# Performance work log

Measured on AMD Instinct MI355X. Metric: run time of the kernel, lower is better.

The kernel has to match this reference:

```python
import jax, jax.numpy as jnp
import numpy as np

DIM = 1024
HEADS = 8
SCALE = 64 ** (-0.5)  # module uses dimHead=64 even though per-head c = DIM//HEADS = 128
LN_EPS = 1e-3  # keras LayerNormalization default


def _layernorm(t, g, b):
    mu = jnp.mean(t, axis=-1, keepdims=True)
    var = jnp.mean(jnp.square(t - mu), axis=-1, keepdims=True)
    return (t - mu) * jax.lax.rsqrt(var + LN_EPS) * g + b


def setup_inputs() -> dict:
    key = jax.random.key(0)
    ks = jax.random.split(key, 4)
    B, N, D = 4, 2048, DIM
    x = jax.random.normal(ks[0], (B, N, D), dtype=jnp.float32)
    w3 = jax.random.normal(ks[1], (D, 3 * D), dtype=jnp.float32) * (1.0 / np.sqrt(D))
    w1 = jax.random.normal(ks[2], (D, 4 * D), dtype=jnp.float32) * (1.0 / np.sqrt(D))
    w2 = jax.random.normal(ks[3], (4 * D, D), dtype=jnp.float32) * (1.0 / np.sqrt(4 * D))
    return {
        "x": x,
        "ln_g": jnp.ones((D,), jnp.float32),
        "ln_b": jnp.zeros((D,), jnp.float32),
        "w3": w3,
        "b3": jnp.zeros((3 * D,), jnp.float32),
        "w1": w1,
        "b1": jnp.zeros((4 * D,), jnp.float32),
        "w2": w2,
        "b2": jnp.zeros((D,), jnp.float32),
    }


def reference(x, ln_g, ln_b, w3, b3, w1, b1, w2, b2):
    B, N, D = x.shape
    H = HEADS
    C = D // H  # per-head channel dim

    # --- attention branch ---
    y = _layernorm(x, ln_g, ln_b)
    qkv = jax.nn.relu(y @ w3 + b3)  # [B, N, 3D] (note: relu on QKV, as in source)
    # einops 'b n (c h i) -> i b h n c' with i=3: last axis factors as (C, H, 3)
    qkv = qkv.reshape(B, N, C, H, 3)
    qkv = jnp.transpose(qkv, (4, 0, 3, 1, 2))  # [3, B, H, N, C]
    q, k, v = qkv[0], qkv[1], qkv[2]
    scores = jnp.einsum("bhqc,bhkc->bhqk", q, k) * SCALE
    attn = jax.nn.softmax(scores, axis=-1)
    o = jnp.einsum("bhqk,bhkc->bhqc", attn, v)  # [B, H, N, C]
    # 'b h n c -> b n (h c)'
    o = jnp.transpose(o, (0, 2, 1, 3)).reshape(B, N, H * C)
    y = o + x

    # --- MLP branch (shared layernorm params; dropout is identity at inference) ---
    y1 = _layernorm(y, ln_g, ln_b)
    mlp = jax.nn.relu(y1 @ w1 + b1) @ w2 + b2
    return mlp + y
```

## Files before the change

### kernel.cpp

```cpp
#include <hip/hip_runtime.h>
#include <hip/hip_bf16.h>
#include <cstdint>

typedef __attribute__((ext_vector_type(8))) __bf16 bf16x8;
typedef __attribute__((ext_vector_type(4))) float f32x4;
typedef unsigned short u16;

#define DEV static __device__ __forceinline__

constexpr float ATT_SCALE = 0.125f;
constexpr float LN_EPS = 1e-3f;

DEV void gload16(const void* g, void* l) {
  __builtin_amdgcn_global_load_lds((__attribute__((address_space(1))) void*)(g),
                                   (__attribute__((address_space(3))) void*)(l),
                                   16, 0, 0);
}

DEV u16 f2b(float f) { __hip_bfloat16 h = __float2bfloat16(f); return __builtin_bit_cast(u16, h); }

template<int PERM>
__global__ __launch_bounds__(256)
void k_transpose(const float* __restrict__ in, __hip_bfloat16* __restrict__ out,
                 int R, int C) {
  __shared__ float t[64][65];
  int d0 = blockIdx.x * 64, k0 = blockIdx.y * 64;
  int tid = threadIdx.x;
  int c64 = tid & 63, r4 = tid >> 6;
#pragma unroll
  for (int i = 0; i < 16; i++) {
    int kr = i * 4 + r4;
    t[c64][kr] = in[(size_t)(k0 + kr) * C + d0 + c64];
  }
  __syncthreads();
#pragma unroll
  for (int i = 0; i < 16; i++) {
    int dr = i * 4 + r4;
    int d = d0 + dr;
    int jp = PERM ? ((d % 3) * 1024 + ((d / 3) & 7) * 128 + (d / 24)) : d;
    out[(size_t)jp * R + k0 + c64] = __float2bfloat16(t[dr][c64]);
  }
}

__global__ __launch_bounds__(256)
void k_ln(const float* __restrict__ in, const float* __restrict__ g,
          const float* __restrict__ b, __hip_bfloat16* __restrict__ out) {
  int row = blockIdx.x, tid = threadIdx.x;
  const float4* in4 = (const float4*)(in + (size_t)row * 1024);
  float4 v = in4[tid];
  float s = v.x + v.y + v.z + v.w;
  float ss = v.x * v.x + v.y * v.y + v.z * v.z + v.w * v.w;
#pragma unroll
  for (int off = 32; off; off >>= 1) { s += __shfl_down(s, off); ss += __shfl_down(ss, off); }
  __shared__ float red[8];
  int w = tid >> 6, lane = tid & 63;
  if (lane == 0) { red[w] = s; red[4 + w] = ss; }
  __syncthreads();
  if (tid == 0) {
    float S = red[0] + red[1] + red[2] + red[3];
    float SS = red[4] + red[5] + red[6] + red[7];
    float mu = S * (1.f / 1024.f);
    float var = SS * (1.f / 1024.f) - mu * mu;
    red[0] = mu; red[1] = rsqrtf(var + LN_EPS);
  }
  __syncthreads();
  float mu = red[0], rs = red[1];
  int c = tid * 4;
  ushort4 o;
  o.x = f2b((v.x - mu) * rs * g[c + 0] + b[c + 0]);
  o.y = f2b((v.y - mu) * rs * g[c + 1] + b[c + 1]);
  o.z = f2b((v.z - mu) * rs * g[c + 2] + b[c + 2]);
  o.w = f2b((v.w - mu) * rs * g[c + 3] + b[c + 3]);
  ((ushort4*)((u16*)out + (size_t)row * 1024))[tid] = o;
}

template<int MODE>
__global__ __launch_bounds__(256, 2)
void k_gemm(const __hip_bfloat16* __restrict__ A,
            const __hip_bfloat16* __restrict__ Bt,
            const float* __restrict__ bias,
            const float* __restrict__ resid,
            float* __restrict__ outF,
            __hip_bfloat16* __restrict__ outQ,
            __hip_bfloat16* __restrict__ outK,
            __hip_bfloat16* __restrict__ outV,
            int K, int Nout) {
  __shared__ alignas(16) __hip_bfloat16 Asm[128 * 32];
  __shared__ alignas(16) __hip_bfloat16 Bsm[128 * 32];
  int tid = threadIdx.x, w = tid >> 6, lane = tid & 63;
  int wr = w >> 1, wc = w & 1;
  int lr = lane >> 4, lc = lane & 15;
  int m0 = blockIdx.y * 128, n0 = blockIdx.x * 128;
  f32x4 acc[4][4] = {};
  const __hip_bfloat16* aG = A + (size_t)(m0 + (tid >> 2)) * K + (tid & 3) * 8;
  const __hip_bfloat16* bG = Bt + (size_t)(n0 + (tid >> 2)) * K + (tid & 3) * 8;
  char* aB = (char*)Asm + w * 1024;
  char* bB = (char*)Bsm + w * 1024;
  for (int k0 = 0; k0 < K; k0 += 32) {
    gload16(aG + k0, aB);
    gload16(aG + (size_t)64 * K + k0, aB + 4096);
    gload16(bG + k0, bB);
    gload16(bG + (size_t)64 * K + k0, bB + 4096);
    __syncthreads();
    bf16x8 af[4], bfr[4];
#pragma unroll
    for (int mi = 0; mi < 4; mi++)
      af[mi] = *(const bf16x8*)(Asm + (wr * 64 + mi * 16 + lc) * 32 + lr * 8);
#pragma unroll
    for (int ni = 0; ni < 4; ni++)
      bfr[ni] = *(const bf16x8*)(Bsm + (wc * 64 + ni * 16 + lc) * 32 + lr * 8);
#pragma unroll
    for (int mi = 0; mi < 4; mi++)
#pragma unroll
      for (int ni = 0; ni < 4; ni++)
        acc[mi][ni] = __builtin_amdgcn_mfma_f32_16x16x32_bf16(af[mi], bfr[ni], acc[mi][ni], 0, 0, 0);
    __syncthreads();
  }
#pragma unroll
  for (int mi = 0; mi < 4; mi++) {
#pragma unroll
    for (int ni = 0; ni < 4; ni++) {
      int jp = n0 + wc * 64 + ni * 16 + lc;
#pragma unroll
      for (int r = 0; r < 4; r++) {
        int m = m0 + wr * 64 + mi * 16 + lr * 4 + r;
        float v = acc[mi][ni][r];
        if (MODE == 0) {
          int i = jp >> 10, h = (jp >> 7) & 7, c = jp & 127;
          v += bias[c * 24 + h * 3 + i];
          v = fmaxf(v, 0.f);
          __hip_bfloat16 bv = __float2bfloat16(v);
          int b_ = m >> 11, n = m & 2047;
          size_t bh = (size_t)(b_ * 8 + h);
          if (i == 0)      outQ[(bh * 2048 + n) * 128 + c] = bv;
          else if (i == 1) outK[(bh * 2048 + n) * 128 + c] = bv;
          else             outV[(bh * 128 + c) * 2048 + n] = bv;
        } else if (MODE == 1) {
          v += bias[jp];
          v = fmaxf(v, 0.f);
          outQ[(size_t)m * Nout + jp] = __float2bfloat16(v);
        } else {
          v += bias[jp] + resid[(size_t)m * Nout + jp];
          outF[(size_t)m * Nout + jp] = v;
        }
      }
    }
  }
}

__global__ __launch_bounds__(512, 4)
void k_attn(const __hip_bfloat16* __restrict__ qb,
            const __hip_bfloat16* __restrict__ kb,
            const __hip_bfloat16* __restrict__ vtb,
            const float* __restrict__ x,
            float* __restrict__ y) {
  __shared__ alignas(16) __hip_bfloat16 Kl[2][64 * 128];
  __shared__ alignas(16) __hip_bfloat16 Vl[128 * 64];
  __shared__ alignas(16) __hip_bfloat16 Pl[8 * 16 * 72];
  int tid = threadIdx.x, w = tid >> 6, lane = tid & 63;
  int lr = lane >> 4, lc = lane & 15;
  int sxz = (lc & 7) << 3;
  int qt = blockIdx.x, bh = blockIdx.y;
  int b_ = bh >> 3, h = bh & 7;
  int q0 = qt * 128;
  size_t bhN = (size_t)bh * 2048;

  bf16x8 qf[4];
#pragma unroll
  for (int ks = 0; ks < 4; ks++)
    qf[ks] = *(const bf16x8*)(qb + (bhN + q0 + w * 16 + lc) * 128 + ks * 32 + lr * 8);

  f32x4 oacc[8] = {};
  float mrun[4], lrun[4];
#pragma unroll
  for (int r = 0; r < 4; r++) { mrun[r] = -1e30f; lrun[r] = 0.f; }

  int krow = tid >> 4;
  int kcol = ((tid & 15) * 8) ^ ((krow & 7) << 3);
  const __hip_bfloat16* kG = kb + (bhN + krow) * 128 + kcol;
  int vrow = tid >> 3;
  int vcol = ((tid & 7) * 8) ^ ((vrow & 7) << 3);
  const __hip_bfloat16* vG = vtb + ((size_t)bh * 128 + vrow) * 2048 + vcol;

  auto STAGE_K = [&](int kv0, int buf) {
    char* kB = (char*)(&Kl[buf][0]) + w * 1024;
#pragma unroll
    for (int p = 0; p < 2; p++)
      gload16(kG + (size_t)(kv0 + p * 32) * 128, kB + p * 8192);
  };
  auto STAGE_V = [&](int kv0) {
    char* vB = (char*)(&Vl[0]) + w * 1024;
#pragma unroll
    for (int p = 0; p < 2; p++)
      gload16(vG + kv0 + (size_t)p * 64 * 2048, vB + p * 8192);
  };

  STAGE_V(0);
  STAGE_K(0, 0);
  asm volatile("s_waitcnt vmcnt(0)" ::: "memory");
  __syncthreads();

  for (int it = 0; it < 32; ++it) {
    int buf = it & 1;
    if (it > 0) STAGE_V(it * 64);
    if (it < 31) STAGE_K((it + 1) * 64, buf ^ 1);
    const __hip_bfloat16* Kb = &Kl[buf][0];

    f32x4 sf[4] = {};
    __builtin_amdgcn_s_setprio(1);
#pragma unroll
    for (int ks = 0; ks < 4; ks++) {
      bf16x8 kfr[4];
#pragma unroll
      for (int ni = 0; ni < 4; ni++)
        kfr[ni] = *(const bf16x8*)(Kb + (ni * 16 + lc) * 128 + ((ks * 32 + lr * 8) ^ sxz));
#pragma unroll
      for (int ni = 0; ni < 4; ni++)
        sf[ni] = __builtin_amdgcn_mfma_f32_16x16x32_bf16(qf[ks], kfr[ni], sf[ni], 0, 0, 0);
    }
    __builtin_amdgcn_s_setprio(0);

    float tmax[4];
    bool need = false;
#pragma unroll
    for (int r = 0; r < 4; r++) {
      float tm = fmaxf(fmaxf(sf[0][r], sf[1][r]), fmaxf(sf[2][r], sf[3][r]));
#pragma unroll
      for (int off = 1; off < 16; off <<= 1) tm = fmaxf(tm, __shfl_xor(tm, off, 16));
      tm *= ATT_SCALE;
      tmax[r] = tm;
      need = need || (tm > mrun[r] + 8.f);
    }
    if (__any(need)) {
#pragma unroll
      for (int r = 0; r < 4; r++) {
        float mnew = fmaxf(mrun[r], tmax[r]);
        float alpha = __expf(mrun[r] - mnew);
        mrun[r] = mnew;
        lrun[r] *= alpha;
#pragma unroll
        for (int nc = 0; nc < 8; nc++) oacc[nc][r] *= alpha;
      }
    }
#pragma unroll
    for (int r = 0; r < 4; r++) {
      float rs = 0.f;
#pragma unroll
      for (int ni = 0; ni < 4; ni++) {
        float p = __expf(sf[ni][r] * ATT_SCALE - mrun[r]);
        sf[ni][r] = p;
        rs += p;
      }
#pragma unroll
      for (int off = 1; off < 16; off <<= 1) rs += __shfl_xor(rs, off, 16);
      lrun[r] += rs;
    }

#pragma unroll
    for (int ni = 0; ni < 4; ni++)
#pragma unroll
      for (int r = 0; r < 4; r++)
        Pl[w * 1152 + (lr * 4 + r) * 72 + ni * 16 + lc] = __float2bfloat16(sf[ni][r]);

    if (it < 31) asm volatile("s_waitcnt vmcnt(2) lgkmcnt(0)" ::: "memory");
    else         asm volatile("s_waitcnt vmcnt(0) lgkmcnt(0)" ::: "memory");
    __builtin_amdgcn_s_barrier();

    __builtin_amdgcn_s_setprio(1);
#pragma unroll
    for (int ks2 = 0; ks2 < 2; ks2++) {
      bf16x8 pa = *(const bf16x8*)(Pl + w * 1152 + lc * 72 + ks2 * 32 + lr * 8);
#pragma unroll
      for (int nc = 0; nc < 8; nc++) {
        bf16x8 vf = *(const bf16x8*)(Vl + (nc * 16 + lc) * 64 + ((ks2 * 32 + lr * 8) ^ sxz));
        oacc[nc] = __builtin_amdgcn_mfma_f32_16x16x32_bf16(pa, vf, oacc[nc], 0, 0, 0);
      }
    }
    __builtin_amdgcn_s_setprio(0);
    __syncthreads();
  }

#pragma unroll
  for (int r = 0; r < 4; r++) {
    int n = q0 + w * 16 + lr * 4 + r;
    float inv = 1.f / lrun[r];
    size_t base = ((size_t)(b_ * 2048 + n)) * 1024 + h * 128;
#pragma unroll
    for (int nc = 0; nc < 8; nc++) {
      int c = nc * 16 + lc;
      y[base + c] = oacc[nc][r] * inv + x[base + c];
    }
  }
}

extern "C" void kernel_launch(void* const* d_in, const int* in_sizes, int n_in,
                              void* d_out, int out_size, void* d_ws, size_t ws_size,
                              hipStream_t stream) {
  const float* x   = (const float*)d_in[0];
  const float* lng = (const float*)d_in[1];
  const float* lnb = (const float*)d_in[2];
  const float* w3  = (const float*)d_in[3];
  const float* b3  = (const float*)d_in[4];
  const float* w1  = (const float*)d_in[5];
  const float* b1  = (const float*)d_in[6];
  const float* w2  = (const float*)d_in[7];
  const float* b2  = (const float*)d_in[8];
  float* out = (float*)d_out;

  constexpr size_t M = 8192;
  __hip_bfloat16* w3t  = (__hip_bfloat16*)d_ws;
  __hip_bfloat16* w1t  = w3t + (size_t)3072 * 1024;
  __hip_bfloat16* w2t  = w1t + (size_t)4096 * 1024;
  __hip_bfloat16* xln  = w2t + (size_t)4096 * 1024;
  __hip_bfloat16* qb   = xln + M * 1024;
  __hip_bfloat16* kbuf = qb + M * 1024;
  __hip_bfloat16* vtb  = kbuf + M * 1024;
  __hip_bfloat16* hmid = qb;

  k_transpose<1><<<dim3(48, 16), 256, 0, stream>>>(w3, w3t, 1024, 3072);
  k_transpose<0><<<dim3(64, 16), 256, 0, stream>>>(w1, w1t, 1024, 4096);
  k_transpose<0><<<dim3(16, 64), 256, 0, stream>>>(w2, w2t, 4096, 1024);
  k_ln<<<dim3(M), 256, 0, stream>>>(x, lng, lnb, xln);
  k_gemm<0><<<dim3(24, 64), 256, 0, stream>>>(xln, w3t, b3, nullptr, nullptr,
                                              qb, kbuf, vtb, 1024, 3072);
  k_attn<<<dim3(16, 32), 512, 0, stream>>>(qb, kbuf, vtb, x, out);
  k_ln<<<dim3(M), 256, 0, stream>>>(out, lng, lnb, xln);
  k_gemm<1><<<dim3(32, 64), 256, 0, stream>>>(xln, w1t, b1, nullptr, nullptr,
                                              hmid, nullptr, nullptr, 1024, 4096);
  k_gemm<2><<<dim3(8, 64), 256, 0, stream>>>(hmid, w2t, b2, out, out,
                                             nullptr, nullptr, nullptr, 4096, 1024);
}
```

Measured before the change: 540.1 us.

## Double-buffer GEMM LDS tiles and compute softmax row sums via MFMA

The GEMM now stages A/B tiles into a two-slot LDS buffer, prefetching the next K-tile while the current one is consumed, so one barrier per iteration replaces two and load latency overlaps MFMA work. MFMA issue in the GEMM also runs at raised wave priority. In attention, the per-row softmax sum is accumulated by an extra MFMA against a ones vector on the bf16 P tile, and the max reduction across lanes is done only when a rescale is needed, removing shuffle reductions. Doubling the GEMM LDS may reduce occupancy, and summing bf16-rounded probabilities slightly changes normalization numerics.

```diff
diff --git a/kernel.cpp b/kernel.cpp
--- a/kernel.cpp
+++ b/kernel.cpp
@@ -85,8 +85,7 @@
             __hip_bfloat16* __restrict__ outK,
             __hip_bfloat16* __restrict__ outV,
             int K, int Nout) {
-  __shared__ alignas(16) __hip_bfloat16 Asm[128 * 32];
-  __shared__ alignas(16) __hip_bfloat16 Bsm[128 * 32];
+  __shared__ alignas(16) __hip_bfloat16 lds[2][2 * 128 * 32];
   int tid = threadIdx.x, w = tid >> 6, lane = tid & 63;
   int wr = w >> 1, wc = w & 1;
   int lr = lane >> 4, lc = lane & 15;
@@ -94,14 +93,26 @@
   f32x4 acc[4][4] = {};
   const __hip_bfloat16* aG = A + (size_t)(m0 + (tid >> 2)) * K + (tid & 3) * 8;
   const __hip_bfloat16* bG = Bt + (size_t)(n0 + (tid >> 2)) * K + (tid & 3) * 8;
-  char* aB = (char*)Asm + w * 1024;
-  char* bB = (char*)Bsm + w * 1024;
-  for (int k0 = 0; k0 < K; k0 += 32) {
-    gload16(aG + k0, aB);
-    gload16(aG + (size_t)64 * K + k0, aB + 4096);
-    gload16(bG + k0, bB);
-    gload16(bG + (size_t)64 * K + k0, bB + 4096);
-    __syncthreads();
+  const size_t K64 = (size_t)64 * K;
+  int NT = K >> 5;
+
+  auto STAGE = [&](int t, int buf) {
+    char* s = (char*)(&lds[buf][0]) + w * 1024;
+    const __hip_bfloat16* ap = aG + t * 32;
+    gload16(ap, s);
+    gload16(ap + K64, s + 4096);
+    const __hip_bfloat16* bp = bG + t * 32;
+    gload16(bp, s + 8192);
+    gload16(bp + K64, s + 12288);
+  };
+
+  STAGE(0, 0);
+  __syncthreads();
+  int cur = 0;
+  for (int t = 0; t < NT; ++t) {
+    if (t + 1 < NT) STAGE(t + 1, cur ^ 1);
+    const __hip_bfloat16* Asm = &lds[cur][0];
+    const __hip_bfloat16* Bsm = &lds[cur][128 * 32];
     bf16x8 af[4], bfr[4];
 #pragma unroll
     for (int mi = 0; mi < 4; mi++)
@@ -109,13 +120,17 @@
 #pragma unroll
     for (int ni = 0; ni < 4; ni++)
       bfr[ni] = *(const bf16x8*)(Bsm + (wc * 64 + ni * 16 + lc) * 32 + lr * 8);
+    __builtin_amdgcn_s_setprio(1);
 #pragma unroll
     for (int mi = 0; mi < 4; mi++)
 #pragma unroll
       for (int ni = 0; ni < 4; ni++)
         acc[mi][ni] = __builtin_amdgcn_mfma_f32_16x16x32_bf16(af[mi], bfr[ni], acc[mi][ni], 0, 0, 0);
+    __builtin_amdgcn_s_setprio(0);
     __syncthreads();
-  }
+    cur ^= 1;
+  }
+
 #pragma unroll
   for (int mi = 0; mi < 4; mi++) {
 #pragma unroll
@@ -165,15 +180,20 @@
   int q0 = qt * 128;
   size_t bhN = (size_t)bh * 2048;
 
+  const u16 one16 = 0x3F80;
+  const __bf16 oneb = __builtin_bit_cast(__bf16, one16);
+  const bf16x8 vones = {oneb, oneb, oneb, oneb, oneb, oneb, oneb, oneb};
+
   bf16x8 qf[4];
 #pragma unroll
   for (int ks = 0; ks < 4; ks++)
     qf[ks] = *(const bf16x8*)(qb + (bhN + q0 + w * 16 + lc) * 128 + ks * 32 + lr * 8);
 
   f32x4 oacc[8] = {};
-  float mrun[4], lrun[4];
-#pragma unroll
-  for (int r = 0; r < 4; r++) { mrun[r] = -1e30f; lrun[r] = 0.f; }
+  f32x4 osum = {};
+  float mrun[4];
+#pragma unroll
+  for (int r = 0; r < 4; r++) mrun[r] = -1e30f;
 
   int krow = tid >> 4;
   int kcol = ((tid & 15) * 8) ^ ((krow & 7) << 3);
@@ -220,41 +240,32 @@
     }
     __builtin_amdgcn_s_setprio(0);
 
-    float tmax[4];
+    float lmax[4];
     bool need = false;
 #pragma unroll
     for (int r = 0; r < 4; r++) {
-      float tm = fmaxf(fmaxf(sf[0][r], sf[1][r]), fmaxf(sf[2][r], sf[3][r]));
-#pragma unroll
-      for (int off = 1; off < 16; off <<= 1) tm = fmaxf(tm, __shfl_xor(tm, off, 16));
-      tm *= ATT_SCALE;
-      tmax[r] = tm;
-      need = need || (tm > mrun[r] + 8.f);
+      lmax[r] = fmaxf(fmaxf(sf[0][r], sf[1][r]), fmaxf(sf[2][r], sf[3][r]));
+      need = need || (lmax[r] * ATT_SCALE > mrun[r] + 8.f);
     }
     if (__any(need)) {
 #pragma unroll
       for (int r = 0; r < 4; r++) {
-        float mnew = fmaxf(mrun[r], tmax[r]);
+        float tm = lmax[r];
+#pragma unroll
+        for (int off = 1; off < 16; off <<= 1) tm = fmaxf(tm, __shfl_xor(tm, off, 16));
+        float mnew = fmaxf(mrun[r], tm * ATT_SCALE);
         float alpha = __expf(mrun[r] - mnew);
         mrun[r] = mnew;
-        lrun[r] *= alpha;
+        osum[r] *= alpha;
 #pragma unroll
         for (int nc = 0; nc < 8; nc++) oacc[nc][r] *= alpha;
       }
     }
 #pragma unroll
-    for (int r = 0; r < 4; r++) {
-      float rs = 0.f;
-#pragma unroll
-      for (int ni = 0; ni < 4; ni++) {
-        float p = __expf(sf[ni][r] * ATT_SCALE - mrun[r]);
-        sf[ni][r] = p;
-        rs += p;
-      }
-#pragma unroll
-      for (int off = 1; off < 16; off <<= 1) rs += __shfl_xor(rs, off, 16);
-      lrun[r] += rs;
-    }
+    for (int r = 0; r < 4; r++)
+#pragma unroll
+      for (int ni = 0; ni < 4; ni++)
+        sf[ni][r] = __expf(sf[ni][r] * ATT_SCALE - mrun[r]);
 
 #pragma unroll
     for (int ni = 0; ni < 4; ni++)
@@ -270,6 +281,7 @@
 #pragma unroll
     for (int ks2 = 0; ks2 < 2; ks2++) {
       bf16x8 pa = *(const bf16x8*)(Pl + w * 1152 + lc * 72 + ks2 * 32 + lr * 8);
+      osum = __builtin_amdgcn_mfma_f32_16x16x32_bf16(pa, vones, osum, 0, 0, 0);
 #pragma unroll
       for (int nc = 0; nc < 8; nc++) {
         bf16x8 vf = *(const bf16x8*)(Vl + (nc * 16 + lc) * 64 + ((ks2 * 32 + lr * 8) ^ sxz));
@@ -283,7 +295,7 @@
 #pragma unroll
   for (int r = 0; r < 4; r++) {
     int n = q0 + w * 16 + lr * 4 + r;
-    float inv = 1.f / lrun[r];
+    float inv = 1.f / osum[r];
     size_t base = ((size_t)(b_ * 2048 + n)) * 1024 + h * 128;
 #pragma unroll
     for (int nc = 0; nc < 8; nc++) {
```

Result: faster. 499.6 us (-7.5%).
